# Optimization experiments

Hardware: AMD Instinct MI355X
Metric: run time of the kernel (lower is better)

The kernel has to match this reference:

```python
import jax, jax.numpy as jnp
import numpy as np

EPS = 1e-6


def setup_inputs() -> dict:
    key = jax.random.key(0)
    ks = jax.random.split(key, 7)
    T, B, D, n, r = 512, 32, 1024, 1024, 8
    x = jax.random.normal(ks[0], (T, B, D), dtype=jnp.float32)
    # xavier_uniform-like init for weights
    def xavier(k, shape):
        fan_in, fan_out = shape[1], shape[0]
        a = float(np.sqrt(6.0 / (fan_in + fan_out)))
        return jax.random.uniform(k, shape, dtype=jnp.float32, minval=-a, maxval=a)
    W_k = xavier(ks[1], (n, D))
    W_v = xavier(ks[2], (n, D))
    W_q = xavier(ks[3], (n, D))
    W_kr = xavier(ks[4], (r, n))
    U0 = jnp.zeros((B, n, r), dtype=jnp.float32)
    V0 = jax.random.normal(ks[5], (B, n, r), dtype=jnp.float32) * 0.01
    return {"x": x, "W_k": W_k, "W_v": W_v, "W_q": W_q, "W_kr": W_kr, "U0": U0, "V0": V0}


def reference(x, W_k, W_v, W_q, W_kr, U0, V0):
    # x: [T, B, D]; state S = U @ V^T with U,V: [B, n, r]
    k = jnp.einsum('tbd,nd->tbn', x, W_k)
    v = jnp.einsum('tbd,nd->tbn', x, W_v)
    q = jnp.einsum('tbd,nd->tbn', x, W_q)
    V = V0  # V is never updated in the recurrence

    def step(U, kvq):
        k_t, v_t, q_t = kvq  # each [B, n]
        k_norm = k_t / (jnp.linalg.norm(k_t, axis=-1, keepdims=True) + EPS)
        Vtk = jnp.einsum('bnr,bn->br', V, k_norm)
        retrieved = jnp.einsum('bnr,br->bn', U, Vtk)
        delta = v_t - retrieved
        k_r = k_norm @ W_kr.T  # [B, r]
        U_new = jnp.tanh(U + delta[:, :, None] * k_r[:, None, :])
        Vtq = jnp.einsum('bnr,bn->br', V, q_t)
        Sq = jnp.einsum('bnr,br->bn', U_new, Vtq)
        out = Sq * jax.nn.silu(Sq)
        return U_new, out

    U_final, output = jax.lax.scan(step, U0, (k, v, q))
    return output, (U_final, V)
```

## Files before the change

### kernel.cpp

```cpp
#include <hip/hip_runtime.h>
#include <hip/hip_bf16.h>

typedef __attribute__((ext_vector_type(8))) short short8;
typedef __attribute__((ext_vector_type(4))) short short4v;
typedef __attribute__((ext_vector_type(4))) float f32x4;
typedef unsigned short u16;

__device__ inline float b2f(u16 u) {
    unsigned int i = ((unsigned int)u) << 16;
    float f; __builtin_memcpy(&f, &i, 4); return f;
}
__device__ inline u16 f2b(float f) {
    unsigned int i; __builtin_memcpy(&i, &f, 4);
    unsigned int r = (i + 0x7FFFu + ((i >> 16) & 1u)) >> 16;
    return (u16)r;
}

__device__ inline float xsum32(float x) {
    unsigned u; __builtin_memcpy(&u, &x, 4);
    auto r = __builtin_amdgcn_permlane32_swap(u, u, false, false);
    unsigned s0 = r[0], s1 = r[1];
    float f0, f1; __builtin_memcpy(&f0, &s0, 4); __builtin_memcpy(&f1, &s1, 4);
    return f0 + f1;
}

#define GLDS(g, l) __builtin_amdgcn_global_load_lds( \
    (const __attribute__((address_space(1))) void*)(g), \
    (__attribute__((address_space(3))) void*)(l), 16, 0, 0)

#define KWAIT(N) asm volatile("s_waitcnt lgkmcnt(0)\n\t" \
                              "s_waitcnt vmcnt(" #N ")\n\t" \
                              "s_barrier" ::: "memory")

__global__ __launch_bounds__(256) void cvt_k(const float* __restrict__ src,
                                             u16* __restrict__ dst, int n4)
{
    const int i = blockIdx.x * blockDim.x + threadIdx.x;
    if (i < n4) {
        const f32x4 v = ((const f32x4*)src)[i];
        short4v o;
        o.x = (short)f2b(v.x); o.y = (short)f2b(v.y);
        o.z = (short)f2b(v.z); o.w = (short)f2b(v.w);
        ((short4v*)dst)[i] = o;
    }
}

__global__ __launch_bounds__(256) void vT_k(const float* __restrict__ V0,
                                            float* __restrict__ V0T)
{
    const int gid = blockIdx.x * 256 + threadIdx.x;
    const int b = gid >> 9, j = (gid >> 6) & 7, n0 = (gid & 63) * 16;
    const float* src = V0 + (long)b * 8192 + (long)n0 * 8 + j;
    float* dst = V0T + (long)b * 8192 + (long)j * 1024 + n0;
#pragma unroll
    for (int i = 0; i < 16; i += 4) {
        f32x4 o = { src[(i + 0) * 8], src[(i + 1) * 8],
                    src[(i + 2) * 8], src[(i + 3) * 8] };
        *(f32x4*)(dst + i) = o;
    }
}

__global__ __launch_bounds__(256) void foldq_k(const float* __restrict__ V0T,
                                               const float* __restrict__ Wq,
                                               float* __restrict__ Aqp)
{
    const int b  = blockIdx.x >> 3;
    const int kc = blockIdx.x & 7;
    const int tid = threadIdx.x;
    const int d0 = tid * 4;

    __shared__ float rs[8][128];
    {
        const int j = tid >> 5, nn = (tid & 31) * 4;
        *(f32x4*)&rs[j][nn] =
            *(const f32x4*)(V0T + (long)b * 8192 + j * 1024 + kc * 128 + nn);
    }
    __syncthreads();

    f32x4 acc[8];
#pragma unroll
    for (int r = 0; r < 8; ++r) acc[r] = (f32x4){0.f, 0.f, 0.f, 0.f};

    const float* wp = Wq + (long)(kc * 128) * 1024 + d0;
#pragma unroll 4
    for (int nb = 0; nb < 32; ++nb) {
        const f32x4 w0 = *(const f32x4*)(wp);
        const f32x4 w1 = *(const f32x4*)(wp + 1024);
        const f32x4 w2 = *(const f32x4*)(wp + 2048);
        const f32x4 w3 = *(const f32x4*)(wp + 3072);
        wp += 4096;
#pragma unroll
        for (int r = 0; r < 8; ++r) {
            const f32x4 rv = *(const f32x4*)&rs[r][nb * 4];
            f32x4 a = acc[r];
            a.x = fmaf(rv.x, w0.x, a.x); a.y = fmaf(rv.x, w0.y, a.y);
            a.z = fmaf(rv.x, w0.z, a.z); a.w = fmaf(rv.x, w0.w, a.w);
            a.x = fmaf(rv.y, w1.x, a.x); a.y = fmaf(rv.y, w1.y, a.y);
            a.z = fmaf(rv.y, w1.z, a.z); a.w = fmaf(rv.y, w1.w, a.w);
            a.x = fmaf(rv.z, w2.x, a.x); a.y = fmaf(rv.z, w2.y, a.y);
            a.z = fmaf(rv.z, w2.z, a.z); a.w = fmaf(rv.z, w2.w, a.w);
            a.x = fmaf(rv.w, w3.x, a.x); a.y = fmaf(rv.w, w3.y, a.y);
            a.z = fmaf(rv.w, w3.z, a.z); a.w = fmaf(rv.w, w3.w, a.w);
            acc[r] = a;
        }
    }

#pragma unroll
    for (int r = 0; r < 8; ++r)
        *(f32x4*)(Aqp + (long)kc * 262144 + (long)(b * 8 + r) * 1024 + d0) = acc[r];
}

__global__ __launch_bounds__(256) void redq_k(const float* __restrict__ Aqp,
                                              float* __restrict__ Aq)
{
    const int i = blockIdx.x * 256 + threadIdx.x;
    f32x4 s = ((const f32x4*)Aqp)[i];
#pragma unroll
    for (int kc = 1; kc < 8; ++kc) {
        const f32x4 p = ((const f32x4*)Aqp)[(long)kc * 65536 + i];
        s.x += p.x; s.y += p.y; s.z += p.z; s.w += p.w;
    }
    ((f32x4*)Aq)[i] = s;
}

__global__ __launch_bounds__(512) void gemm256_kv(
    const u16* __restrict__ Xbf, const u16* __restrict__ Wbf,
    u16* __restrict__ Ko, u16* __restrict__ Vo)
{
    __shared__ u16 lds[65536];

    const int bid = blockIdx.x;
    const int swz = (bid & 7) * 64 + (bid >> 3);
    const int bm = swz >> 3, bnx = swz & 7;
    const int widx = bnx >> 2;
    const int nbase = (bnx & 3) * 256;
    const int m0 = bm * 256;
    const u16* Wp = Wbf + (long)widx * 1048576;
    u16* O = (widx == 0) ? Ko : Vo;

    const int tid = threadIdx.x;
    const int w = tid >> 6;
    const int lane = tid & 63;
    const int wm = (w >> 2) * 128;
    const int wn = (w & 3) * 64;
    const int ln = lane & 15, qd = lane >> 4;

    const int q8 = lane >> 3, s8 = lane & 7;
    const int cc = s8 ^ q8;
    const u16* p0; const u16* p1; const u16* p2; const u16* p3;
    {
        auto mk = [&](int l) -> const u16* {
            const int r = l * 64 + w * 8 + q8;
            return (cc < 4)
                ? (Xbf + (long)(m0 + r) * 1024 + cc * 8)
                : (Wp  + (long)(nbase + r) * 1024 + (cc - 4) * 8);
        };
        p0 = mk(0); p1 = mk(1); p2 = mk(2); p3 = mk(3);
    }

    int aoff[8], boff[4];
#pragma unroll
    for (int mf = 0; mf < 8; ++mf) {
        const int ro = wm + mf * 16 + ln;
        aoff[mf] = ro * 128 + ((qd ^ (ro & 7)) * 16);
    }
#pragma unroll
    for (int nf = 0; nf < 4; ++nf) {
        const int rb = wn + nf * 16 + ln;
        boff[nf] = rb * 128 + (((4 + qd) ^ (rb & 7)) * 16);
    }

    f32x4 acc[8][4];
#pragma unroll
    for (int i = 0; i < 8; ++i)
#pragma unroll
        for (int j = 0; j < 4; ++j) acc[i][j] = (f32x4){0.f, 0.f, 0.f, 0.f};

#pragma unroll
    for (int tt = 0; tt < 3; ++tt) {
        char* db = (char*)lds + tt * 32768 + w * 1024;
        GLDS(p0, db);
        GLDS(p1, db + 8192);
        GLDS(p2, db + 16384);
        GLDS(p3, db + 24576);
        p0 += 32; p1 += 32; p2 += 32; p3 += 32;
    }
    KWAIT(8);

    for (int t = 0; t < 32; ++t) {
        const char* bb = (const char*)lds + (t & 3) * 32768;
        short8 a[8], bfr[4];
#pragma unroll
        for (int mf = 0; mf < 4; ++mf) a[mf] = *(const short8*)(bb + aoff[mf]);
#pragma unroll
        for (int nf = 0; nf < 4; ++nf) bfr[nf] = *(const short8*)(bb + boff[nf]);
        if (t < 29) {
            char* db = (char*)lds + ((t + 3) & 3) * 32768 + w * 1024;
            GLDS(p0, db);
            GLDS(p1, db + 8192);
            p0 += 32; p1 += 32;
        }
        __builtin_amdgcn_s_setprio(1);
#pragma unroll
        for (int mf = 0; mf < 4; ++mf)
#pragma unroll
            for (int nf = 0; nf < 4; ++nf)
                acc[mf][nf] = __builtin_amdgcn_mfma_f32_16x16x32_bf16(
                    a[mf], bfr[nf], acc[mf][nf], 0, 0, 0);
        __builtin_amdgcn_s_setprio(0);
#pragma unroll
        for (int mf = 4; mf < 8; ++mf) a[mf] = *(const short8*)(bb + aoff[mf]);
        if (t < 29) {
            char* db = (char*)lds + ((t + 3) & 3) * 32768 + w * 1024;
            GLDS(p2, db + 16384);
            GLDS(p3, db + 24576);
            p2 += 32; p3 += 32;
        }
        __builtin_amdgcn_s_setprio(1);
#pragma unroll
        for (int mf = 4; mf < 8; ++mf)
#pragma unroll
            for (int nf = 0; nf < 4; ++nf)
                acc[mf][nf] = __builtin_amdgcn_mfma_f32_16x16x32_bf16(
                    a[mf], bfr[nf], acc[mf][nf], 0, 0, 0);
        __builtin_amdgcn_s_setprio(0);
        if (t < 29)       KWAIT(8);
        else if (t == 29) KWAIT(4);
        else if (t == 30) KWAIT(0);
    }

#pragma unroll
    for (int mf = 0; mf < 8; ++mf) {
#pragma unroll
        for (int nf = 0; nf < 4; ++nf) {
            const int r0 = m0 + wm + mf * 16 + qd * 4;
            const int c  = nbase + wn + nf * 16 + ln;
#pragma unroll
            for (int r = 0; r < 4; ++r)
                O[(long)(r0 + r) * 1024 + c] = f2b(acc[mf][nf][r]);
        }
    }
}

__global__ __launch_bounds__(256) void scal_k(
    const u16* __restrict__ K, const u16* __restrict__ X,
    const float* __restrict__ V0T, const float* __restrict__ Wkr,
    const float* __restrict__ Aq, float* __restrict__ S)
{
    const int b  = blockIdx.x & 31;
    const int t0 = (blockIdx.x >> 5) * 4;
    const int tid = threadIdx.x;
    const int j = tid & 7, c = tid >> 3;
    const int n0 = c * 32;

    f32x4 vv[8], ww[8], aqv[8];
    {
        const f32x4* vp = (const f32x4*)(V0T + (long)b * 8192 + (long)j * 1024 + n0);
        const f32x4* wp = (const f32x4*)(Wkr + (long)j * 1024 + n0);
        const f32x4* ap = (const f32x4*)(Aq + (long)(b * 8 + j) * 1024 + n0);
#pragma unroll
        for (int i = 0; i < 8; i++) { vv[i] = vp[i]; ww[i] = wp[i]; aqv[i] = ap[i]; }
    }

    float avk[4], akr[4], avq[4], ass[4];
#pragma unroll
    for (int dt = 0; dt < 4; dt++) { avk[dt] = akr[dt] = avq[dt] = ass[dt] = 0.f; }

#pragma unroll
    for (int dt = 0; dt < 4; dt++) {
        const long m = (long)(t0 + dt) * 32 + b;
        const short8* kp = (const short8*)(K + m * 1024 + n0);
        const short8* xp = (const short8*)(X + m * 1024 + n0);
#pragma unroll
        for (int i = 0; i < 4; i++) {
            const short8 kb = kp[i], xb = xp[i];
#pragma unroll
            for (int e = 0; e < 8; e++) {
                const int idx = i * 8 + e;
                const float kv = b2f((u16)kb[e]);
                const float xv = b2f((u16)xb[e]);
                const float vj = vv[idx >> 2][idx & 3];
                const float wj = ww[idx >> 2][idx & 3];
                const float aj = aqv[idx >> 2][idx & 3];
                avk[dt] = fmaf(vj, kv, avk[dt]);
                akr[dt] = fmaf(wj, kv, akr[dt]);
                avq[dt] = fmaf(aj, xv, avq[dt]);
                ass[dt] = fmaf(kv, kv, ass[dt]);
            }
        }
    }

    __shared__ float red[4][4][3][8];
    __shared__ float ssr[4][4];
    const int wave = tid >> 6, lane = tid & 63;
#pragma unroll
    for (int dt = 0; dt < 4; dt++) {
        float a = avk[dt], k2 = akr[dt], q = avq[dt], s = ass[dt];
#pragma unroll
        for (int off = 8; off < 64; off <<= 1) {
            a  += __shfl_xor(a,  off, 64);
            k2 += __shfl_xor(k2, off, 64);
            q  += __shfl_xor(q,  off, 64);
            s  += __shfl_xor(s,  off, 64);
        }
        if (lane < 8) {
            red[wave][dt][0][lane] = a;
            red[wave][dt][1][lane] = k2;
            red[wave][dt][2][lane] = q;
        }
        if (lane == 0) ssr[wave][dt] = s;
    }
    __syncthreads();
    if (tid < 128) {
        const int dt = tid >> 5, rr = tid & 31;
        if (rr < 24) {
            const int v = rr >> 3, jj = rr & 7;
            float s = red[0][dt][v][jj] + red[1][dt][v][jj] +
                      red[2][dt][v][jj] + red[3][dt][v][jj];
            if (v != 2) {
                const float n2 = ssr[0][dt] + ssr[1][dt] + ssr[2][dt] + ssr[3][dt];
                const float inv = 1.0f / (sqrtf(n2) + 1e-6f);
                s *= (v == 0) ? (0.5f * inv) : (2.0f * inv);
            } else {
                s *= 0.5f;
            }
            S[((long)b * 512 + t0 + dt) * 32 + v * 8 + jj] = s;
        }
    }
}

__global__ __launch_bounds__(128) void scan_k(
    const u16* __restrict__ Vbuf, const float* __restrict__ S,
    const float* __restrict__ U0, float* __restrict__ outp,
    float* __restrict__ Ufin)
{
    __shared__ float Sl[512 * 32];

    const int b = blockIdx.x >> 4;
    const int chunk = blockIdx.x & 15;
    const int wave = threadIdx.x >> 6, lane = threadIdx.x & 63;
    const int rh = lane >> 5;
    const int n = chunk * 64 + wave * 32 + (lane & 31);
    const int so = rh * 4;

    {
        const f32x4* Sg = (const f32x4*)(S + (long)b * 16384);
        f32x4* Sd = (f32x4*)Sl;
        for (int i = threadIdx.x; i < 4096; i += 128) Sd[i] = Sg[i];
    }

    float U[4];
    {
        const float* u0 = U0 + ((long)b * 1024 + n) * 8 + so;
#pragma unroll
        for (int j2 = 0; j2 < 4; j2++) U[j2] = 2.0f * u0[j2];
    }

    const u16* vp0 = Vbuf + (long)b * 1024 + n;
    u16 vnx[16];
#pragma unroll
    for (int i = 0; i < 16; i++) vnx[i] = vp0[(long)i * 32768];

    __syncthreads();

    f32x4 sb[4][3];
#pragma unroll
    for (int s = 0; s < 4; ++s)
#pragma unroll
        for (int r = 0; r < 3; ++r)
            sb[s][r] = *(const f32x4*)&Sl[s * 32 + r * 8 + so];

    float* op = outp + (long)b * 1024 + n;

    for (int t0 = 0; t0 < 512; t0 += 16) {
        float vcur[16];
#pragma unroll
        for (int i = 0; i < 16; i++) vcur[i] = b2f(vnx[i]);
        const int tn = (t0 + 16 < 512) ? (t0 + 16) : t0;
#pragma unroll
        for (int i = 0; i < 16; i++) vnx[i] = vp0[(long)(tn + i) * 32768];

#pragma unroll
        for (int i = 0; i < 16; i++) {
            const int t = t0 + i;
            const int slot = i & 3;
            const f32x4 a = sb[slot][0], Kk = sb[slot][1], Qq = sb[slot][2];

            float pr = fmaf(U[0], a.x, U[1] * a.y) + fmaf(U[2], a.z, U[3] * a.w);
            const float ret = xsum32(pr);
            const float delta = vcur[i] - ret;

            const float kr4[4] = {Kk.x, Kk.y, Kk.z, Kk.w};
            const float vq4[4] = {Qq.x, Qq.y, Qq.z, Qq.w};

            float sq0 = 0.f, sq1 = 0.f;
#pragma unroll
            for (int j2 = 0; j2 < 4; j2++) {
                const float xx = fmaf(delta, kr4[j2], U[j2]);
                const float e = __expf(xx);
                const float rc = __builtin_amdgcn_rcpf(e + 1.0f);
                const float u = fmaf(-4.0f, rc, 2.0f);
                U[j2] = u;
                if (j2 & 1) sq1 = fmaf(u, vq4[j2], sq1);
                else        sq0 = fmaf(u, vq4[j2], sq0);
            }

            const int tf = (t + 4 < 512) ? (t + 4) : 511;
#pragma unroll
            for (int r = 0; r < 3; r++)
                sb[slot][r] = *(const f32x4*)&Sl[tf * 32 + r * 8 + so];

            const float Sq = xsum32(sq0 + sq1);
            const float sg = __builtin_amdgcn_rcpf(1.0f + __expf(-Sq));
            const float o = Sq * Sq * sg;
            if (rh == 0) op[(long)t * 32768] = o;
        }
    }

    *(f32x4*)(Ufin + ((long)b * 1024 + n) * 8 + so) =
        (f32x4){0.5f * U[0], 0.5f * U[1], 0.5f * U[2], 0.5f * U[3]};
}

__global__ __launch_bounds__(256) void vcopy_k(const float* __restrict__ src,
                                               float* __restrict__ dst)
{
    const int i = blockIdx.x * blockDim.x + threadIdx.x;
    ((f32x4*)dst)[i] = ((const f32x4*)src)[i];
}

extern "C" void kernel_launch(void* const* d_in, const int* in_sizes, int n_in,
                              void* d_out, int out_size, void* d_ws, size_t ws_size,
                              hipStream_t stream)
{
    const float* x   = (const float*)d_in[0];
    const float* Wk  = (const float*)d_in[1];
    const float* Wv  = (const float*)d_in[2];
    const float* Wq  = (const float*)d_in[3];
    const float* Wkr = (const float*)d_in[4];
    const float* U0  = (const float*)d_in[5];
    const float* V0  = (const float*)d_in[6];
    float* out = (float*)d_out;

    char* ws = (char*)d_ws;
    u16*   Xbf = (u16*)(ws);
    u16*   Wbf = (u16*)(ws + 33554432);
    u16*   Kb  = (u16*)(ws + 39845888);
    u16*   Vb  = (u16*)(ws + 73400320);
    float* Aq  = (float*)(ws + 106954752);
    float* Aqp = (float*)(ws + 108003328);
    float* Sc  = (float*)(ws + 140509184);
    float* V0T = (float*)(ws + 142606336);

    cvt_k<<<16384, 256, 0, stream>>>(x,  Xbf,               4194304);
    cvt_k<<<1024,  256, 0, stream>>>(Wk, Wbf,                262144);
    cvt_k<<<1024,  256, 0, stream>>>(Wv, Wbf + 1048576,      262144);
    vT_k <<<64,    256, 0, stream>>>(V0, V0T);
    foldq_k<<<256, 256, 0, stream>>>(V0T, Wq, Aqp);
    redq_k <<<256, 256, 0, stream>>>(Aqp, Aq);

    gemm256_kv<<<512, 512, 0, stream>>>(Xbf, Wbf, Kb, Vb);
    scal_k  <<<4096, 256, 0, stream>>>(Kb, Xbf, V0T, Wkr, Aq, Sc);
    scan_k  <<<512, 128, 0, stream>>>(Vb, Sc, U0, out, out + 16777216);
    vcopy_k <<<256, 256, 0, stream>>>(V0, out + 17039360);
}
```

Measured before the change: 425.1 us.

## Split scan rank across four lane groups and widen foldq grid

The scan kernel now spreads each row's 8 rank components over four 16-lane groups (2 per lane) instead of two 32-lane halves. It uses 256 threads per block and reads the per-step scalars straight from global memory with an 8-deep register prefetch, where before it staged them in a 64KB LDS tile. This halves the serial transcendental work per lane on the latency-bound recurrence, at the cost of an extra cross-lane permute per reduction. The foldq kernel is also split four ways along d with scalar loads, to fill more CUs.

```diff
diff --git a/kernel.cpp b/kernel.cpp
--- a/kernel.cpp
+++ b/kernel.cpp
@@ -4,6 +4,7 @@
 typedef __attribute__((ext_vector_type(8))) short short8;
 typedef __attribute__((ext_vector_type(4))) short short4v;
 typedef __attribute__((ext_vector_type(4))) float f32x4;
+typedef __attribute__((ext_vector_type(2))) float f32x2;
 typedef unsigned short u16;
 
 __device__ inline float b2f(u16 u) {
@@ -22,6 +23,18 @@
     unsigned s0 = r[0], s1 = r[1];
     float f0, f1; __builtin_memcpy(&f0, &s0, 4); __builtin_memcpy(&f1, &s1, 4);
     return f0 + f1;
+}
+
+__device__ inline float xsum16(float x) {
+#if __has_builtin(__builtin_amdgcn_permlane16_swap)
+    unsigned u; __builtin_memcpy(&u, &x, 4);
+    auto r = __builtin_amdgcn_permlane16_swap(u, u, false, false);
+    unsigned s0 = r[0], s1 = r[1];
+    float f0, f1; __builtin_memcpy(&f0, &s0, 4); __builtin_memcpy(&f1, &s1, 4);
+    return f0 + f1;
+#else
+    return x + __shfl_xor(x, 16, 64);
+#endif
 }
 
 #define GLDS(g, l) __builtin_amdgcn_global_load_lds( \
@@ -64,10 +77,12 @@
                                                const float* __restrict__ Wq,
                                                float* __restrict__ Aqp)
 {
-    const int b  = blockIdx.x >> 3;
-    const int kc = blockIdx.x & 7;
+    const int bid = blockIdx.x;
+    const int b  = bid >> 5;
+    const int kc = (bid >> 2) & 7;
+    const int dg = bid & 3;
     const int tid = threadIdx.x;
-    const int d0 = tid * 4;
+    const int d = dg * 256 + tid;
 
     __shared__ float rs[8][128];
     {
@@ -77,37 +92,33 @@
     }
     __syncthreads();
 
-    f32x4 acc[8];
-#pragma unroll
-    for (int r = 0; r < 8; ++r) acc[r] = (f32x4){0.f, 0.f, 0.f, 0.f};
-
-    const float* wp = Wq + (long)(kc * 128) * 1024 + d0;
+    float acc[8];
+#pragma unroll
+    for (int r = 0; r < 8; ++r) acc[r] = 0.f;
+
+    const float* wp = Wq + (long)(kc * 128) * 1024 + d;
 #pragma unroll 4
     for (int nb = 0; nb < 32; ++nb) {
-        const f32x4 w0 = *(const f32x4*)(wp);
-        const f32x4 w1 = *(const f32x4*)(wp + 1024);
-        const f32x4 w2 = *(const f32x4*)(wp + 2048);
-        const f32x4 w3 = *(const f32x4*)(wp + 3072);
+        const float w0 = wp[0];
+        const float w1 = wp[1024];
+        const float w2 = wp[2048];
+        const float w3 = wp[3072];
         wp += 4096;
 #pragma unroll
         for (int r = 0; r < 8; ++r) {
             const f32x4 rv = *(const f32x4*)&rs[r][nb * 4];
-            f32x4 a = acc[r];
-            a.x = fmaf(rv.x, w0.x, a.x); a.y = fmaf(rv.x, w0.y, a.y);
-            a.z = fmaf(rv.x, w0.z, a.z); a.w = fmaf(rv.x, w0.w, a.w);
-            a.x = fmaf(rv.y, w1.x, a.x); a.y = fmaf(rv.y, w1.y, a.y);
-            a.z = fmaf(rv.y, w1.z, a.z); a.w = fmaf(rv.y, w1.w, a.w);
-            a.x = fmaf(rv.z, w2.x, a.x); a.y = fmaf(rv.z, w2.y, a.y);
-            a.z = fmaf(rv.z, w2.z, a.z); a.w = fmaf(rv.z, w2.w, a.w);
-            a.x = fmaf(rv.w, w3.x, a.x); a.y = fmaf(rv.w, w3.y, a.y);
-            a.z = fmaf(rv.w, w3.z, a.z); a.w = fmaf(rv.w, w3.w, a.w);
+            float a = acc[r];
+            a = fmaf(rv.x, w0, a);
+            a = fmaf(rv.y, w1, a);
+            a = fmaf(rv.z, w2, a);
+            a = fmaf(rv.w, w3, a);
             acc[r] = a;
         }
     }
 
 #pragma unroll
     for (int r = 0; r < 8; ++r)
-        *(f32x4*)(Aqp + (long)kc * 262144 + (long)(b * 8 + r) * 1024 + d0) = acc[r];
+        Aqp[(long)kc * 262144 + (long)(b * 8 + r) * 1024 + d] = acc[r];
 }
 
 __global__ __launch_bounds__(256) void redq_k(const float* __restrict__ Aqp,
@@ -329,31 +340,24 @@
     }
 }
 
-__global__ __launch_bounds__(128) void scan_k(
+__global__ __launch_bounds__(256) void scan_k(
     const u16* __restrict__ Vbuf, const float* __restrict__ S,
     const float* __restrict__ U0, float* __restrict__ outp,
     float* __restrict__ Ufin)
 {
-    __shared__ float Sl[512 * 32];
-
     const int b = blockIdx.x >> 4;
     const int chunk = blockIdx.x & 15;
     const int wave = threadIdx.x >> 6, lane = threadIdx.x & 63;
-    const int rh = lane >> 5;
-    const int n = chunk * 64 + wave * 32 + (lane & 31);
-    const int so = rh * 4;
-
-    {
-        const f32x4* Sg = (const f32x4*)(S + (long)b * 16384);
-        f32x4* Sd = (f32x4*)Sl;
-        for (int i = threadIdx.x; i < 4096; i += 128) Sd[i] = Sg[i];
-    }
-
-    float U[4];
+    const int rq = lane >> 4;
+    const int nl = lane & 15;
+    const int n = chunk * 64 + wave * 16 + nl;
+    const int so = rq * 2;
+
+    float U[2];
     {
         const float* u0 = U0 + ((long)b * 1024 + n) * 8 + so;
-#pragma unroll
-        for (int j2 = 0; j2 < 4; j2++) U[j2] = 2.0f * u0[j2];
+        U[0] = 2.0f * u0[0];
+        U[1] = 2.0f * u0[1];
     }
 
     const u16* vp0 = Vbuf + (long)b * 1024 + n;
@@ -361,14 +365,13 @@
 #pragma unroll
     for (int i = 0; i < 16; i++) vnx[i] = vp0[(long)i * 32768];
 
-    __syncthreads();
-
-    f32x4 sb[4][3];
-#pragma unroll
-    for (int s = 0; s < 4; ++s)
-#pragma unroll
-        for (int r = 0; r < 3; ++r)
-            sb[s][r] = *(const f32x4*)&Sl[s * 32 + r * 8 + so];
+    const float* Sp = S + (long)b * 16384 + so;
+    f32x2 sb[8][3];
+#pragma unroll
+    for (int s = 0; s < 8; ++s)
+#pragma unroll
+        for (int v = 0; v < 3; ++v)
+            sb[s][v] = *(const f32x2*)(Sp + s * 32 + v * 8);
 
     float* op = outp + (long)b * 1024 + n;
 
@@ -383,42 +386,37 @@
 #pragma unroll
         for (int i = 0; i < 16; i++) {
             const int t = t0 + i;
-            const int slot = i & 3;
-            const f32x4 a = sb[slot][0], Kk = sb[slot][1], Qq = sb[slot][2];
-
-            float pr = fmaf(U[0], a.x, U[1] * a.y) + fmaf(U[2], a.z, U[3] * a.w);
-            const float ret = xsum32(pr);
+            const int slot = i & 7;
+            const f32x2 a = sb[slot][0], Kk = sb[slot][1], Qq = sb[slot][2];
+
+            const float pr = fmaf(U[0], a.x, U[1] * a.y);
+            const float ret = xsum32(xsum16(pr));
             const float delta = vcur[i] - ret;
 
-            const float kr4[4] = {Kk.x, Kk.y, Kk.z, Kk.w};
-            const float vq4[4] = {Qq.x, Qq.y, Qq.z, Qq.w};
-
-            float sq0 = 0.f, sq1 = 0.f;
-#pragma unroll
-            for (int j2 = 0; j2 < 4; j2++) {
-                const float xx = fmaf(delta, kr4[j2], U[j2]);
-                const float e = __expf(xx);
-                const float rc = __builtin_amdgcn_rcpf(e + 1.0f);
-                const float u = fmaf(-4.0f, rc, 2.0f);
-                U[j2] = u;
-                if (j2 & 1) sq1 = fmaf(u, vq4[j2], sq1);
-                else        sq0 = fmaf(u, vq4[j2], sq0);
-            }
-
-            const int tf = (t + 4 < 512) ? (t + 4) : 511;
-#pragma unroll
-            for (int r = 0; r < 3; r++)
-                sb[slot][r] = *(const f32x4*)&Sl[tf * 32 + r * 8 + so];
-
-            const float Sq = xsum32(sq0 + sq1);
+            const float x0 = fmaf(delta, Kk.x, U[0]);
+            const float x1 = fmaf(delta, Kk.y, U[1]);
+            const float e0 = __expf(x0);
+            const float e1 = __expf(x1);
+            const float u0n = fmaf(-4.0f, __builtin_amdgcn_rcpf(e0 + 1.0f), 2.0f);
+            const float u1n = fmaf(-4.0f, __builtin_amdgcn_rcpf(e1 + 1.0f), 2.0f);
+            U[0] = u0n; U[1] = u1n;
+
+            const float sqp = fmaf(u1n, Qq.y, u0n * Qq.x);
+
+            const int tf = (t + 8 < 512) ? (t + 8) : 511;
+#pragma unroll
+            for (int v = 0; v < 3; ++v)
+                sb[slot][v] = *(const f32x2*)(Sp + tf * 32 + v * 8);
+
+            const float Sq = xsum32(xsum16(sqp));
             const float sg = __builtin_amdgcn_rcpf(1.0f + __expf(-Sq));
             const float o = Sq * Sq * sg;
-            if (rh == 0) op[(long)t * 32768] = o;
-        }
-    }
-
-    *(f32x4*)(Ufin + ((long)b * 1024 + n) * 8 + so) =
-        (f32x4){0.5f * U[0], 0.5f * U[1], 0.5f * U[2], 0.5f * U[3]};
+            if (rq == 0) op[(long)t * 32768] = o;
+        }
+    }
+
+    *(f32x2*)(Ufin + ((long)b * 1024 + n) * 8 + so) =
+        (f32x2){0.5f * U[0], 0.5f * U[1]};
 }
 
 __global__ __launch_bounds__(256) void vcopy_k(const float* __restrict__ src,
@@ -455,11 +453,11 @@
     cvt_k<<<1024,  256, 0, stream>>>(Wk, Wbf,                262144);
     cvt_k<<<1024,  256, 0, stream>>>(Wv, Wbf + 1048576,      262144);
     vT_k <<<64,    256, 0, stream>>>(V0, V0T);
-    foldq_k<<<256, 256, 0, stream>>>(V0T, Wq, Aqp);
+    foldq_k<<<1024, 256, 0, stream>>>(V0T, Wq, Aqp);
     redq_k <<<256, 256, 0, stream>>>(Aqp, Aq);
 
     gemm256_kv<<<512, 512, 0, stream>>>(Xbf, Wbf, Kb, Vb);
     scal_k  <<<4096, 256, 0, stream>>>(Kb, Xbf, V0T, Wkr, Aq, Sc);
-    scan_k  <<<512, 128, 0, stream>>>(Vb, Sc, U0, out, out + 16777216);
+    scan_k  <<<512, 256, 0, stream>>>(Vb, Sc, U0, out, out + 16777216);
     vcopy_k <<<256, 256, 0, stream>>>(V0, out + 17039360);
 }
```

After: 425.4 us. Within noise of the previous version (+0.1%).
